# Optimization experiments

Measured on AMD Instinct MI355X. Metric: run time of the kernel, lower is better.

## Reference

```python
import jax, jax.numpy as jnp
import numpy as np

B, S, D = 4, 2048, 1024
E = 8            # num_experts
H = 2 * D        # int(4*D*(1/top_k)) with top_k=2, scaling_factor='auto'


def setup_inputs() -> dict:
    key = jax.random.key(0)
    ks = jax.random.split(key, 8)
    sd = 1.0 / np.sqrt(D)
    sh = 1.0 / np.sqrt(H)
    return {
        "x": jax.random.normal(ks[0], (B, S, D), dtype=jnp.float32),
        "top_k": 2,
        "Wg": jax.random.uniform(ks[1], (D, E), jnp.float32, -sd, sd),
        "bg": jax.random.uniform(ks[2], (E,), jnp.float32, -sd, sd),
        "W1": jax.random.uniform(ks[3], (E, D, H), jnp.float32, -sd, sd),
        "b1": jax.random.uniform(ks[4], (E, H), jnp.float32, -sd, sd),
        "W2": jax.random.uniform(ks[5], (E, H, D), jnp.float32, -sh, sh),
        "b2": jax.random.uniform(ks[6], (E, D), jnp.float32, -sh, sh),
    }


def reference(x, top_k, Wg, bg, W1, b1, W2, b2):
    b, s, d = x.shape
    e = W1.shape[0]
    T = b * s
    xt = x.reshape(T, d)                                   # [T, D]
    gate_logits = xt @ Wg + bg                             # [T, E]
    gate_probas = jax.nn.softmax(gate_logits, axis=-1)
    topk_p, topk_i = jax.lax.top_k(gate_probas, top_k)     # [T, K]
    topk_p = topk_p / jnp.sum(topk_p, axis=-1, keepdims=True)
    # combine weights per expert: zero for unselected experts
    w = jnp.zeros((T, e), dtype=x.dtype).at[jnp.arange(T)[:, None], topk_i].add(topk_p)  # [T, E]
    # dense grouped FFN over experts; unselected experts are zero-weighted,
    # so the weighted combine matches the original gather-MLP-scatter math
    h = jax.nn.gelu(jnp.einsum('td,edh->teh', xt, W1) + b1, approximate=True)  # [T, E, H]
    y = jnp.einsum('teh,ehd->ted', h, W2) + b2             # [T, E, D]
    out = jnp.einsum('te,ted->td', w, y)                   # [T, D]
    return out.reshape(b, s, d)
```

## Files before the change

### kernel.cpp

```cpp
#include <hip/hip_runtime.h>

typedef unsigned short u16;
typedef short v8s __attribute__((ext_vector_type(8)));
typedef float v4f __attribute__((ext_vector_type(4)));
typedef u16 u16x8 __attribute__((ext_vector_type(8)));
typedef u16 u16x4 __attribute__((ext_vector_type(4)));

constexpr int Tn = 8192;
constexpr int Dd = 1024;
constexpr int Hh = 2048;
constexpr int Ee = 8;
constexpr int MAXP = 17;

static __device__ __forceinline__ u16 f2bf(float v) {
  unsigned u = __float_as_uint(v);
  unsigned r = (u + 0x7fffu + ((u >> 16) & 1u)) >> 16;
  return (u16)r;
}

static __device__ __forceinline__ float bf2f(u16 v) {
  return __uint_as_float(((unsigned)v) << 16);
}

static __device__ __forceinline__ void gload_lds16(const u16* g, u16* l) {
  __builtin_amdgcn_global_load_lds(
      (const __attribute__((address_space(1))) unsigned int*)g,
      (__attribute__((address_space(3))) unsigned int*)l, 16, 0, 0);
}


__global__ __launch_bounds__(256) void prep_kernel(
    const float* __restrict__ x, const float* __restrict__ Wg, const float* __restrict__ bg,
    int* __restrict__ topki, float* __restrict__ topkw, u16* __restrict__ xb,
    const float* __restrict__ W1, u16* __restrict__ w1t,
    const float* __restrict__ W2, u16* __restrict__ w2t) {
  __shared__ float tile[64][65];
  int blk = blockIdx.x;

  if (blk < 2048) {
    int lane = threadIdx.x & 63;
    int t = blk * 4 + (threadIdx.x >> 6);
    const float4* xr = reinterpret_cast<const float4*>(x + (size_t)t * Dd);
    float acc[8] = {0.f, 0.f, 0.f, 0.f, 0.f, 0.f, 0.f, 0.f};
#pragma unroll
    for (int it = 0; it < 4; ++it) {
      float4 xv = xr[it * 64 + lane];
      int r = it * 256 + lane * 4;
      ushort4 o;
      o.x = f2bf(xv.x); o.y = f2bf(xv.y); o.z = f2bf(xv.z); o.w = f2bf(xv.w);
      *reinterpret_cast<ushort4*>(xb + (size_t)t * Dd + r) = o;
      const float4* wr = reinterpret_cast<const float4*>(Wg + (size_t)r * 8);
      float xs[4] = {xv.x, xv.y, xv.z, xv.w};
#pragma unroll
      for (int q = 0; q < 4; ++q) {
        float4 a = wr[q * 2], b = wr[q * 2 + 1];
        acc[0] += xs[q] * a.x; acc[1] += xs[q] * a.y; acc[2] += xs[q] * a.z; acc[3] += xs[q] * a.w;
        acc[4] += xs[q] * b.x; acc[5] += xs[q] * b.y; acc[6] += xs[q] * b.z; acc[7] += xs[q] * b.w;
      }
    }
#pragma unroll
    for (int e = 0; e < 8; ++e) {
#pragma unroll
      for (int off = 32; off > 0; off >>= 1) acc[e] += __shfl_xor(acc[e], off, 64);
    }
    if (lane == 0) {
      float l[8];
      float mx = -1e30f;
#pragma unroll
      for (int e = 0; e < 8; ++e) { l[e] = acc[e] + bg[e]; mx = fmaxf(mx, l[e]); }
      int i0 = 0;
#pragma unroll
      for (int e = 1; e < 8; ++e) if (l[e] > l[i0]) i0 = e;
      int i1 = (i0 == 0) ? 1 : 0;
#pragma unroll
      for (int e = 0; e < 8; ++e) if (e != i0 && l[e] > l[i1]) i1 = e;
      float e0 = __expf(l[i0] - mx), e1 = __expf(l[i1] - mx);
      float inv = 1.0f / (e0 + e1);
      topki[2 * t] = i0; topki[2 * t + 1] = i1;
      topkw[2 * t] = e0 * inv; topkw[2 * t + 1] = e1 * inv;
    }
    return;
  }

  int b = blk - 2048;
  bool isW1 = b < 4096;
  const float* in;
  u16* out;
  int R, C, cx, cy, e;
  if (isW1) {
    e = b >> 9;
    int t = b & 511;
    R = Dd; C = Hh; cx = t & 31; cy = t >> 5;
    in = W1; out = w1t;
  } else {
    int bb = b - 4096;
    e = bb >> 9;
    int t = bb & 511;
    R = Hh; C = Dd; cx = t & 15; cy = t >> 4;
    in = W2; out = w2t;
  }
  const float* ip = in + (size_t)e * Dd * Hh;
  u16* op = out + (size_t)e * Dd * Hh;
  int c0 = cx * 64, r0 = cy * 64;
  int tid = threadIdx.x;

#pragma unroll
  for (int k = 0; k < 4; ++k) {
    int f = k * 256 + tid;
    int r = f >> 4, c4 = (f & 15) * 4;
    float4 v = *reinterpret_cast<const float4*>(ip + (size_t)(r0 + r) * C + c0 + c4);
    tile[r][c4] = v.x; tile[r][c4 + 1] = v.y; tile[r][c4 + 2] = v.z; tile[r][c4 + 3] = v.w;
  }
  __syncthreads();

  int j = tid & 7;
#pragma unroll
  for (int rr = 0; rr < 2; ++rr) {
    int oc = (tid >> 3) + rr * 32;
    u16x8 o;
    if (isW1) {
#pragma unroll
      for (int q = 0; q < 8; ++q) o[q] = f2bf(tile[j * 8 + q][oc]);
    } else {
#pragma unroll
      for (int q = 0; q < 8; ++q) {
        int p = j * 8 + q;
        int src = (p & 3) * 16 + (p >> 2);
        o[q] = f2bf(tile[src][oc]);
      }
    }
    *reinterpret_cast<u16x8*>(op + (size_t)(c0 + oc) * R + r0 + j * 8) = o;
  }
}

__global__ __launch_bounds__(512) void sort_kernel(
    const int* __restrict__ topki,
    int* __restrict__ offs, int* __restrict__ rows, int* __restrict__ slotmap,
    int* __restrict__ panelE, int* __restrict__ panelB, int* __restrict__ nPanels) {
  __shared__ int scan[8][512];
  __shared__ int tot_l[8];
  __shared__ int offs_l[9];
  const int tt = threadIdx.x;
  const int base = tt * 32;

  int ev[32];
  int cnt[8] = {0, 0, 0, 0, 0, 0, 0, 0};
#pragma unroll
  for (int jj = 0; jj < 32; ++jj) {
    int e = topki[base + jj];
    ev[jj] = e;
#pragma unroll
    for (int q = 0; q < 8; ++q) cnt[q] += (e == q) ? 1 : 0;
  }
#pragma unroll
  for (int q = 0; q < 8; ++q) scan[q][tt] = cnt[q];
  __syncthreads();

  {
    int w = tt >> 6, l = tt & 63;
    int v[8];
    int s = 0;
#pragma unroll
    for (int jj = 0; jj < 8; ++jj) { v[jj] = scan[w][l * 8 + jj]; s += v[jj]; }
    int si = s;
#pragma unroll
    for (int off = 1; off < 64; off <<= 1) {
      int o = __shfl_up(si, off, 64);
      if (l >= off) si += o;
    }
    int run = si - s;
#pragma unroll
    for (int jj = 0; jj < 8; ++jj) { scan[w][l * 8 + jj] = run; run += v[jj]; }
    if (l == 63) tot_l[w] = si;
  }
  __syncthreads();

  if (tt == 0) {
    int o = 0;
#pragma unroll
    for (int e = 0; e < 8; ++e) { offs_l[e] = o; o += tot_l[e]; }
    offs_l[8] = o;
#pragma unroll
    for (int e = 0; e < 9; ++e) offs[e] = offs_l[e];
    int np = 0;
    for (int e = 0; e < 8; ++e) {
      for (int m0 = 0; m0 < tot_l[e]; m0 += 128) {
        panelE[np] = e;
        panelB[np] = offs_l[e] + m0;
        ++np;
      }
    }
    *nPanels = np;
  }
  __syncthreads();

#pragma unroll
  for (int jj = 0; jj < 32; ++jj) {
    int e = ev[jj];
    int idx = base + jj;
    int slot = scan[e][tt]++;
    slot += offs_l[e];
    rows[slot] = idx >> 1;
    slotmap[idx] = slot;
  }
}


__global__ __launch_bounds__(256, 2) void gemm1_kernel(
    const u16* __restrict__ xb, const u16* __restrict__ w1t, const float* __restrict__ b1,
    const int* __restrict__ offs, const int* __restrict__ rows,
    const int* __restrict__ panelE, const int* __restrict__ panelB,
    const int* __restrict__ nPanels, u16* __restrict__ hbuf) {
  const int bid = blockIdx.x;
  const int xcd = bid & 7;
  const int q = bid >> 3;
  const int n = q & 15;
  const int pi = (q >> 4) * 8 + xcd;
  if (pi >= *nPanels) return;
  const int e = panelE[pi];
  const int sbase = panelB[pi];
  const int lim = offs[e + 1];
  const int n0 = n * 128;

  __shared__ u16 As[128 * 64];
  __shared__ u16 Bs[128 * 64];

  const int tid = threadIdx.x;
  const int lane = tid & 63;
  const int wid = tid >> 6;
  const int wm = (wid >> 1) * 64;
  const int wn = (wid & 1) * 64;
  const int l16 = lane & 15;
  const int quad = lane >> 4;
  const int swz8 = (l16 & 7) * 8;

  const u16* aga[4];
  const u16* bga[4];
  u16* alds[4];
  u16* blds[4];
  const int lr = lane >> 3;
  const int g = (lane & 7) ^ (lr & 7);
  const int kcol = g * 8;
#pragma unroll
  for (int j = 0; j < 4; ++j) {
    int chunk = wid * 4 + j;
    int rowl = chunk * 8 + lr;
    int slot = sbase + rowl;
    if (slot >= lim) slot = sbase;
    aga[j] = xb + (size_t)rows[slot] * Dd + kcol;
    bga[j] = w1t + ((size_t)e * Hh + n0 + rowl) * Dd + kcol;
    alds[j] = As + chunk * 512;
    blds[j] = Bs + chunk * 512;
  }

  v4f acc[4][4];
#pragma unroll
  for (int i = 0; i < 4; ++i)
#pragma unroll
    for (int j = 0; j < 4; ++j) acc[i][j] = {0.f, 0.f, 0.f, 0.f};

  int rowAoff[4], rowBoff[4];
#pragma unroll
  for (int t_ = 0; t_ < 4; ++t_) {
    rowAoff[t_] = (wm + t_ * 16 + l16) * 64;
    rowBoff[t_] = (wn + t_ * 16 + l16) * 64;
  }

  for (int k0 = 0; k0 < Dd; k0 += 64) {
    __syncthreads();
#pragma unroll
    for (int j = 0; j < 4; ++j) gload_lds16(aga[j] + k0, alds[j]);
#pragma unroll
    for (int j = 0; j < 4; ++j) gload_lds16(bga[j] + k0, blds[j]);
    __syncthreads();

#pragma unroll
    for (int s = 0; s < 2; ++s) {
      int coff = ((s * 4 + quad) * 8) ^ swz8;
      v8s a[4], b[4];
#pragma unroll
      for (int mt = 0; mt < 4; ++mt)
        a[mt] = *reinterpret_cast<const v8s*>(&As[rowAoff[mt] + coff]);
#pragma unroll
      for (int nt = 0; nt < 4; ++nt)
        b[nt] = *reinterpret_cast<const v8s*>(&Bs[rowBoff[nt] + coff]);
#pragma unroll
      for (int mt = 0; mt < 4; ++mt)
#pragma unroll
        for (int nt = 0; nt < 4; ++nt)
          acc[mt][nt] = __builtin_amdgcn_mfma_f32_16x16x32_bf16(a[mt], b[nt], acc[mt][nt], 0, 0, 0);
    }
  }

  float b1v[4];
  const int ngbase = n0 + wn;
#pragma unroll
  for (int nt = 0; nt < 4; ++nt) b1v[nt] = b1[(size_t)e * Hh + ngbase + nt * 16 + l16];
#pragma unroll
  for (int mt = 0; mt < 4; ++mt) {
#pragma unroll
    for (int i = 0; i < 4; ++i) {
      int m = wm + mt * 16 + quad * 4 + i;
      if (sbase + m < lim) {
        u16x4 o;
#pragma unroll
        for (int nt = 0; nt < 4; ++nt) {
          float v = acc[mt][nt][i] + b1v[nt];
          float s = 1.0f / (1.0f + __expf(-1.5957691216057308f * (v + 0.044715f * v * v * v)));
          o[nt] = f2bf(v * s);
        }
        *reinterpret_cast<u16x4*>(hbuf + (size_t)(sbase + m) * Hh + ngbase + l16 * 4) = o;
      }
    }
  }
}

__global__ __launch_bounds__(256, 2) void gemm2_kernel(
    const u16* __restrict__ hbuf, const u16* __restrict__ w2t, const float* __restrict__ b2,
    const int* __restrict__ offs,
    const int* __restrict__ panelE, const int* __restrict__ panelB,
    const int* __restrict__ nPanels, u16* __restrict__ ybuf) {
  const int bid = blockIdx.x;
  const int xcd = bid & 7;
  const int q = bid >> 3;
  const int n = q & 7;
  const int pi = (q >> 3) * 8 + xcd;
  if (pi >= *nPanels) return;
  const int e = panelE[pi];
  const int sbase = panelB[pi];
  const int lim = offs[e + 1];
  const int n0 = n * 128;

  __shared__ u16 As[128 * 64];
  __shared__ u16 Bs[128 * 64];

  const int tid = threadIdx.x;
  const int lane = tid & 63;
  const int wid = tid >> 6;
  const int wm = (wid >> 1) * 64;
  const int wn = (wid & 1) * 64;
  const int l16 = lane & 15;
  const int quad = lane >> 4;
  const int swz8 = (l16 & 7) * 8;

  const u16* aga[4];
  const u16* bga[4];
  u16* alds[4];
  u16* blds[4];
  const int lr = lane >> 3;
  const int g = (lane & 7) ^ (lr & 7);
  const int kcol = g * 8;
#pragma unroll
  for (int j = 0; j < 4; ++j) {
    int chunk = wid * 4 + j;
    int rowl = chunk * 8 + lr;
    int slot = sbase + rowl;
    if (slot >= lim) slot = sbase;
    aga[j] = hbuf + (size_t)slot * Hh + kcol;
    bga[j] = w2t + ((size_t)e * Dd + n0 + rowl) * Hh + kcol;
    alds[j] = As + chunk * 512;
    blds[j] = Bs + chunk * 512;
  }

  v4f acc[4][4];
#pragma unroll
  for (int i = 0; i < 4; ++i)
#pragma unroll
    for (int j = 0; j < 4; ++j) acc[i][j] = {0.f, 0.f, 0.f, 0.f};

  int rowAoff[4], rowBoff[4];
#pragma unroll
  for (int t_ = 0; t_ < 4; ++t_) {
    rowAoff[t_] = (wm + t_ * 16 + l16) * 64;
    rowBoff[t_] = (wn + t_ * 16 + l16) * 64;
  }

  for (int k0 = 0; k0 < Hh; k0 += 64) {
    __syncthreads();
#pragma unroll
    for (int j = 0; j < 4; ++j) gload_lds16(aga[j] + k0, alds[j]);
#pragma unroll
    for (int j = 0; j < 4; ++j) gload_lds16(bga[j] + k0, blds[j]);
    __syncthreads();

#pragma unroll
    for (int s = 0; s < 2; ++s) {
      int coff = ((s * 4 + quad) * 8) ^ swz8;
      v8s a[4], b[4];
#pragma unroll
      for (int mt = 0; mt < 4; ++mt)
        a[mt] = *reinterpret_cast<const v8s*>(&As[rowAoff[mt] + coff]);
#pragma unroll
      for (int nt = 0; nt < 4; ++nt)
        b[nt] = *reinterpret_cast<const v8s*>(&Bs[rowBoff[nt] + coff]);
#pragma unroll
      for (int mt = 0; mt < 4; ++mt)
#pragma unroll
        for (int nt = 0; nt < 4; ++nt)
          acc[mt][nt] = __builtin_amdgcn_mfma_f32_16x16x32_bf16(a[mt], b[nt], acc[mt][nt], 0, 0, 0);
    }
  }

  float b2v[4];
  int ng[4];
#pragma unroll
  for (int nt = 0; nt < 4; ++nt) {
    ng[nt] = n0 + wn + nt * 16 + l16;
    b2v[nt] = b2[(size_t)e * Dd + ng[nt]];
  }
#pragma unroll
  for (int mt = 0; mt < 4; ++mt) {
#pragma unroll
    for (int i = 0; i < 4; ++i) {
      int m = wm + mt * 16 + quad * 4 + i;
      if (sbase + m < lim) {
        size_t rowbase = (size_t)(sbase + m) * Dd;
#pragma unroll
        for (int nt = 0; nt < 4; ++nt)
          ybuf[rowbase + ng[nt]] = f2bf(acc[mt][nt][i] + b2v[nt]);
      }
    }
  }
}

__global__ __launch_bounds__(256) void combine_kernel(
    const u16* __restrict__ ybuf, const int* __restrict__ slotmap,
    const float* __restrict__ topkw, float* __restrict__ out) {
  int idx = blockIdx.x * 256 + threadIdx.x;
  int t = idx >> 7;
  int d0 = (idx & 127) * 8;
  int s0 = slotmap[2 * t], s1 = slotmap[2 * t + 1];
  float w0 = topkw[2 * t], w1 = topkw[2 * t + 1];
  uint4 ya = *reinterpret_cast<const uint4*>(ybuf + (size_t)s0 * Dd + d0);
  uint4 yb = *reinterpret_cast<const uint4*>(ybuf + (size_t)s1 * Dd + d0);
  float r[8];
  const unsigned* pa = &ya.x;
  const unsigned* pb = &yb.x;
#pragma unroll
  for (int j = 0; j < 4; ++j) {
    unsigned a = pa[j], b = pb[j];
    r[2 * j]     = w0 * bf2f((u16)(a & 0xffff)) + w1 * bf2f((u16)(b & 0xffff));
    r[2 * j + 1] = w0 * bf2f((u16)(a >> 16))    + w1 * bf2f((u16)(b >> 16));
  }
  float4* op = reinterpret_cast<float4*>(out + (size_t)t * Dd + d0);
  op[0] = make_float4(r[0], r[1], r[2], r[3]);
  op[1] = make_float4(r[4], r[5], r[6], r[7]);
}

extern "C" void kernel_launch(void* const* d_in, const int* in_sizes, int n_in,
                              void* d_out, int out_size, void* d_ws, size_t ws_size,
                              hipStream_t stream) {
  const float* x  = (const float*)d_in[0];
  const float* Wg = (const float*)d_in[2];
  const float* bg = (const float*)d_in[3];
  const float* W1 = (const float*)d_in[4];
  const float* b1 = (const float*)d_in[5];
  const float* W2 = (const float*)d_in[6];
  const float* b2 = (const float*)d_in[7];
  float* out = (float*)d_out;

  char* p = (char*)d_ws;
  auto take = [&](size_t bytes) {
    char* q = p;
    p += (bytes + 255) & ~(size_t)255;
    return q;
  };
  int*   offs       = (int*)take(64);
  int*   panelE     = (int*)take(1024);
  int*   panelB     = (int*)take(1024);
  int*   nPanels    = (int*)take(256);
  int*   topki      = (int*)take((size_t)Tn * 2 * sizeof(int));
  float* topkw      = (float*)take((size_t)Tn * 2 * sizeof(float));
  int*   rows       = (int*)take((size_t)Tn * 2 * sizeof(int));
  int*   slotmap    = (int*)take((size_t)Tn * 2 * sizeof(int));
  u16*   xb         = (u16*)take((size_t)Tn * Dd * 2);
  u16*   w1t        = (u16*)take((size_t)Ee * Dd * Hh * 2);
  u16*   w2t        = (u16*)take((size_t)Ee * Dd * Hh * 2);
  u16*   hbuf       = (u16*)take((size_t)Tn * 2 * Hh * 2);
  u16*   ybuf       = (u16*)take((size_t)Tn * 2 * Dd * 2);

  prep_kernel<<<10240, 256, 0, stream>>>(x, Wg, bg, topki, topkw, xb, W1, w1t, W2, w2t);
  sort_kernel<<<1, 512, 0, stream>>>(topki, offs, rows, slotmap, panelE, panelB, nPanels);
  gemm1_kernel<<<8 * 16 * MAXP, 256, 0, stream>>>(xb, w1t, b1, offs, rows,
                                                  panelE, panelB, nPanels, hbuf);
  gemm2_kernel<<<8 * 8 * MAXP, 256, 0, stream>>>(hbuf, w2t, b2, offs,
                                                 panelE, panelB, nPanels, ybuf);
  combine_kernel<<<(Tn * Dd / 8) / 256, 256, 0, stream>>>(ybuf, slotmap, topkw, out);
}
```

Baseline: 428.6 us.

## Overlap W2 transpose with GEMM1 and scatter GEMM2 output to token order

```diff
diff --git a/kernel.cpp b/kernel.cpp
--- a/kernel.cpp
+++ b/kernel.cpp
@@ -11,6 +11,8 @@
 constexpr int Hh = 2048;
 constexpr int Ee = 8;
 constexpr int MAXP = 17;
+constexpr int G1GEMM = 8 * 16 * MAXP;
+constexpr int G1XTRA = 1024;
 
 static __device__ __forceinline__ u16 f2bf(float v) {
   unsigned u = __float_as_uint(v);
@@ -29,81 +31,10 @@
 }
 
 
-__global__ __launch_bounds__(256) void prep_kernel(
-    const float* __restrict__ x, const float* __restrict__ Wg, const float* __restrict__ bg,
-    int* __restrict__ topki, float* __restrict__ topkw, u16* __restrict__ xb,
-    const float* __restrict__ W1, u16* __restrict__ w1t,
-    const float* __restrict__ W2, u16* __restrict__ w2t) {
-  __shared__ float tile[64][65];
-  int blk = blockIdx.x;
-
-  if (blk < 2048) {
-    int lane = threadIdx.x & 63;
-    int t = blk * 4 + (threadIdx.x >> 6);
-    const float4* xr = reinterpret_cast<const float4*>(x + (size_t)t * Dd);
-    float acc[8] = {0.f, 0.f, 0.f, 0.f, 0.f, 0.f, 0.f, 0.f};
-#pragma unroll
-    for (int it = 0; it < 4; ++it) {
-      float4 xv = xr[it * 64 + lane];
-      int r = it * 256 + lane * 4;
-      ushort4 o;
-      o.x = f2bf(xv.x); o.y = f2bf(xv.y); o.z = f2bf(xv.z); o.w = f2bf(xv.w);
-      *reinterpret_cast<ushort4*>(xb + (size_t)t * Dd + r) = o;
-      const float4* wr = reinterpret_cast<const float4*>(Wg + (size_t)r * 8);
-      float xs[4] = {xv.x, xv.y, xv.z, xv.w};
-#pragma unroll
-      for (int q = 0; q < 4; ++q) {
-        float4 a = wr[q * 2], b = wr[q * 2 + 1];
-        acc[0] += xs[q] * a.x; acc[1] += xs[q] * a.y; acc[2] += xs[q] * a.z; acc[3] += xs[q] * a.w;
-        acc[4] += xs[q] * b.x; acc[5] += xs[q] * b.y; acc[6] += xs[q] * b.z; acc[7] += xs[q] * b.w;
-      }
-    }
-#pragma unroll
-    for (int e = 0; e < 8; ++e) {
-#pragma unroll
-      for (int off = 32; off > 0; off >>= 1) acc[e] += __shfl_xor(acc[e], off, 64);
-    }
-    if (lane == 0) {
-      float l[8];
-      float mx = -1e30f;
-#pragma unroll
-      for (int e = 0; e < 8; ++e) { l[e] = acc[e] + bg[e]; mx = fmaxf(mx, l[e]); }
-      int i0 = 0;
-#pragma unroll
-      for (int e = 1; e < 8; ++e) if (l[e] > l[i0]) i0 = e;
-      int i1 = (i0 == 0) ? 1 : 0;
-#pragma unroll
-      for (int e = 0; e < 8; ++e) if (e != i0 && l[e] > l[i1]) i1 = e;
-      float e0 = __expf(l[i0] - mx), e1 = __expf(l[i1] - mx);
-      float inv = 1.0f / (e0 + e1);
-      topki[2 * t] = i0; topki[2 * t + 1] = i1;
-      topkw[2 * t] = e0 * inv; topkw[2 * t + 1] = e1 * inv;
-    }
-    return;
-  }
-
-  int b = blk - 2048;
-  bool isW1 = b < 4096;
-  const float* in;
-  u16* out;
-  int R, C, cx, cy, e;
-  if (isW1) {
-    e = b >> 9;
-    int t = b & 511;
-    R = Dd; C = Hh; cx = t & 31; cy = t >> 5;
-    in = W1; out = w1t;
-  } else {
-    int bb = b - 4096;
-    e = bb >> 9;
-    int t = bb & 511;
-    R = Hh; C = Dd; cx = t & 15; cy = t >> 4;
-    in = W2; out = w2t;
-  }
-  const float* ip = in + (size_t)e * Dd * Hh;
-  u16* op = out + (size_t)e * Dd * Hh;
-  int c0 = cx * 64, r0 = cy * 64;
+static __device__ __forceinline__ void transpose_tile64(
+    const float* __restrict__ ip, u16* __restrict__ op,
+    int R, int C, int r0, int c0, bool permute, float (*tile)[65]) {
   int tid = threadIdx.x;
-
 #pragma unroll
   for (int k = 0; k < 4; ++k) {
     int f = k * 256 + tid;
@@ -112,20 +43,19 @@
     tile[r][c4] = v.x; tile[r][c4 + 1] = v.y; tile[r][c4 + 2] = v.z; tile[r][c4 + 3] = v.w;
   }
   __syncthreads();
-
   int j = tid & 7;
 #pragma unroll
   for (int rr = 0; rr < 2; ++rr) {
     int oc = (tid >> 3) + rr * 32;
     u16x8 o;
-    if (isW1) {
+    if (!permute) {
 #pragma unroll
       for (int q = 0; q < 8; ++q) o[q] = f2bf(tile[j * 8 + q][oc]);
     } else {
 #pragma unroll
       for (int q = 0; q < 8; ++q) {
-        int p = j * 8 + q;
-        int src = (p & 3) * 16 + (p >> 2);
+        int p_ = j * 8 + q;
+        int src = (p_ & 3) * 16 + (p_ >> 2);
         o[q] = f2bf(tile[src][oc]);
       }
     }
@@ -133,9 +63,69 @@
   }
 }
 
+__global__ __launch_bounds__(256) void prep_kernel(
+    const float* __restrict__ x, const float* __restrict__ Wg, const float* __restrict__ bg,
+    int* __restrict__ topki, float* __restrict__ topkw, u16* __restrict__ xb,
+    const float* __restrict__ W1, u16* __restrict__ w1t) {
+  __shared__ float tile[64][65];
+  int blk = blockIdx.x;
+
+  if (blk < 4096) {
+    int e = blk >> 9;
+    int t = blk & 511;
+    int cx = t & 31, cy = t >> 5;
+    const float* ip = W1 + (size_t)e * Dd * Hh;
+    u16* op = w1t + (size_t)e * Dd * Hh;
+    transpose_tile64(ip, op, Dd, Hh, cy * 64, cx * 64, false, tile);
+    return;
+  }
+
+  int lane = threadIdx.x & 63;
+  int t = (blk - 4096) * 4 + (threadIdx.x >> 6);
+  const float4* xr = reinterpret_cast<const float4*>(x + (size_t)t * Dd);
+  float acc[8] = {0.f, 0.f, 0.f, 0.f, 0.f, 0.f, 0.f, 0.f};
+#pragma unroll
+  for (int it = 0; it < 4; ++it) {
+    float4 xv = xr[it * 64 + lane];
+    int r = it * 256 + lane * 4;
+    ushort4 o;
+    o.x = f2bf(xv.x); o.y = f2bf(xv.y); o.z = f2bf(xv.z); o.w = f2bf(xv.w);
+    *reinterpret_cast<ushort4*>(xb + (size_t)t * Dd + r) = o;
+    const float4* wr = reinterpret_cast<const float4*>(Wg + (size_t)r * 8);
+    float xs[4] = {xv.x, xv.y, xv.z, xv.w};
+#pragma unroll
+    for (int q = 0; q < 4; ++q) {
+      float4 a = wr[q * 2], b = wr[q * 2 + 1];
+      acc[0] += xs[q] * a.x; acc[1] += xs[q] * a.y; acc[2] += xs[q] * a.z; acc[3] += xs[q] * a.w;
+      acc[4] += xs[q] * b.x; acc[5] += xs[q] * b.y; acc[6] += xs[q] * b.z; acc[7] += xs[q] * b.w;
+    }
+  }
+#pragma unroll
+  for (int e = 0; e < 8; ++e) {
+#pragma unroll
+    for (int off = 32; off > 0; off >>= 1) acc[e] += __shfl_xor(acc[e], off, 64);
+  }
+  if (lane == 0) {
+    float l[8];
+    float mx = -1e30f;
+#pragma unroll
+    for (int e = 0; e < 8; ++e) { l[e] = acc[e] + bg[e]; mx = fmaxf(mx, l[e]); }
+    int i0 = 0;
+#pragma unroll
+    for (int e = 1; e < 8; ++e) if (l[e] > l[i0]) i0 = e;
+    int i1 = (i0 == 0) ? 1 : 0;
+#pragma unroll
+    for (int e = 0; e < 8; ++e) if (e != i0 && l[e] > l[i1]) i1 = e;
+    float e0 = __expf(l[i0] - mx), e1 = __expf(l[i1] - mx);
+    float inv = 1.0f / (e0 + e1);
+    topki[2 * t] = i0; topki[2 * t + 1] = i1;
+    topkw[2 * t] = e0 * inv; topkw[2 * t + 1] = e1 * inv;
+  }
+}
+
 __global__ __launch_bounds__(512) void sort_kernel(
     const int* __restrict__ topki,
-    int* __restrict__ offs, int* __restrict__ rows, int* __restrict__ slotmap,
+    int* __restrict__ offs, int* __restrict__ rows,
     int* __restrict__ panelE, int* __restrict__ panelB, int* __restrict__ nPanels) {
   __shared__ int scan[8][512];
   __shared__ int tot_l[8];
@@ -198,10 +188,8 @@
   for (int jj = 0; jj < 32; ++jj) {
     int e = ev[jj];
     int idx = base + jj;
-    int slot = scan[e][tt]++;
-    slot += offs_l[e];
-    rows[slot] = idx >> 1;
-    slotmap[idx] = slot;
+    int slot = scan[e][tt]++ + offs_l[e];
+    rows[slot] = idx;
   }
 }
 
@@ -210,8 +198,29 @@
     const u16* __restrict__ xb, const u16* __restrict__ w1t, const float* __restrict__ b1,
     const int* __restrict__ offs, const int* __restrict__ rows,
     const int* __restrict__ panelE, const int* __restrict__ panelB,
-    const int* __restrict__ nPanels, u16* __restrict__ hbuf) {
+    const int* __restrict__ nPanels, u16* __restrict__ hbuf,
+    const float* __restrict__ W2, u16* __restrict__ w2t) {
+  __shared__ __align__(16) u16 smem[2 * 128 * 64];
+  u16* As = smem;
+  u16* Bs = smem + 128 * 64;
+
   const int bid = blockIdx.x;
+  if (bid >= G1GEMM) {
+    float (*tile)[65] = reinterpret_cast<float (*)[65]>(smem);
+    int tb = bid - G1GEMM;
+#pragma unroll 1
+    for (int s = 0; s < 4; ++s) {
+      int tileid = tb * 4 + s;
+      int e = tileid >> 9;
+      int t = tileid & 511;
+      int cx = t & 15, cy = t >> 4;
+      if (s) __syncthreads();
+      transpose_tile64(W2 + (size_t)e * Dd * Hh, w2t + (size_t)e * Dd * Hh,
+                       Hh, Dd, cy * 64, cx * 64, true, tile);
+    }
+    return;
+  }
+
   const int xcd = bid & 7;
   const int q = bid >> 3;
   const int n = q & 15;
@@ -222,9 +231,6 @@
   const int lim = offs[e + 1];
   const int n0 = n * 128;
 
-  __shared__ u16 As[128 * 64];
-  __shared__ u16 Bs[128 * 64];
-
   const int tid = threadIdx.x;
   const int lane = tid & 63;
   const int wid = tid >> 6;
@@ -247,7 +253,7 @@
     int rowl = chunk * 8 + lr;
     int slot = sbase + rowl;
     if (slot >= lim) slot = sbase;
-    aga[j] = xb + (size_t)rows[slot] * Dd + kcol;
+    aga[j] = xb + (size_t)(rows[slot] >> 1) * Dd + kcol;
     bga[j] = w1t + ((size_t)e * Hh + n0 + rowl) * Dd + kcol;
     alds[j] = As + chunk * 512;
     blds[j] = Bs + chunk * 512;
@@ -317,7 +323,7 @@
 
 __global__ __launch_bounds__(256, 2) void gemm2_kernel(
     const u16* __restrict__ hbuf, const u16* __restrict__ w2t, const float* __restrict__ b2,
-    const int* __restrict__ offs,
+    const int* __restrict__ offs, const int* __restrict__ rows,
     const int* __restrict__ panelE, const int* __restrict__ panelB,
     const int* __restrict__ nPanels, u16* __restrict__ ybuf) {
   const int bid = blockIdx.x;
@@ -331,8 +337,9 @@
   const int lim = offs[e + 1];
   const int n0 = n * 128;
 
-  __shared__ u16 As[128 * 64];
-  __shared__ u16 Bs[128 * 64];
+  __shared__ __align__(16) u16 smem[2 * 128 * 64];
+  u16* As = smem;
+  u16* Bs = smem + 128 * 64;
 
   const int tid = threadIdx.x;
   const int lane = tid & 63;
@@ -414,7 +421,7 @@
     for (int i = 0; i < 4; ++i) {
       int m = wm + mt * 16 + quad * 4 + i;
       if (sbase + m < lim) {
-        size_t rowbase = (size_t)(sbase + m) * Dd;
+        size_t rowbase = (size_t)rows[sbase + m] * Dd;
 #pragma unroll
         for (int nt = 0; nt < 4; ++nt)
           ybuf[rowbase + ng[nt]] = f2bf(acc[mt][nt][i] + b2v[nt]);
@@ -424,15 +431,14 @@
 }
 
 __global__ __launch_bounds__(256) void combine_kernel(
-    const u16* __restrict__ ybuf, const int* __restrict__ slotmap,
-    const float* __restrict__ topkw, float* __restrict__ out) {
+    const u16* __restrict__ ybuf, const float* __restrict__ topkw,
+    float* __restrict__ out) {
   int idx = blockIdx.x * 256 + threadIdx.x;
   int t = idx >> 7;
   int d0 = (idx & 127) * 8;
-  int s0 = slotmap[2 * t], s1 = slotmap[2 * t + 1];
   float w0 = topkw[2 * t], w1 = topkw[2 * t + 1];
-  uint4 ya = *reinterpret_cast<const uint4*>(ybuf + (size_t)s0 * Dd + d0);
-  uint4 yb = *reinterpret_cast<const uint4*>(ybuf + (size_t)s1 * Dd + d0);
+  uint4 ya = *reinterpret_cast<const uint4*>(ybuf + (size_t)(2 * t) * Dd + d0);
+  uint4 yb = *reinterpret_cast<const uint4*>(ybuf + (size_t)(2 * t + 1) * Dd + d0);
   float r[8];
   const unsigned* pa = &ya.x;
   const unsigned* pb = &yb.x;
@@ -472,18 +478,18 @@
   int*   topki      = (int*)take((size_t)Tn * 2 * sizeof(int));
   float* topkw      = (float*)take((size_t)Tn * 2 * sizeof(float));
   int*   rows       = (int*)take((size_t)Tn * 2 * sizeof(int));
-  int*   slotmap    = (int*)take((size_t)Tn * 2 * sizeof(int));
   u16*   xb         = (u16*)take((size_t)Tn * Dd * 2);
   u16*   w1t        = (u16*)take((size_t)Ee * Dd * Hh * 2);
   u16*   w2t        = (u16*)take((size_t)Ee * Dd * Hh * 2);
   u16*   hbuf       = (u16*)take((size_t)Tn * 2 * Hh * 2);
   u16*   ybuf       = (u16*)take((size_t)Tn * 2 * Dd * 2);
 
-  prep_kernel<<<10240, 256, 0, stream>>>(x, Wg, bg, topki, topkw, xb, W1, w1t, W2, w2t);
-  sort_kernel<<<1, 512, 0, stream>>>(topki, offs, rows, slotmap, panelE, panelB, nPanels);
-  gemm1_kernel<<<8 * 16 * MAXP, 256, 0, stream>>>(xb, w1t, b1, offs, rows,
-                                                  panelE, panelB, nPanels, hbuf);
-  gemm2_kernel<<<8 * 8 * MAXP, 256, 0, stream>>>(hbuf, w2t, b2, offs,
+  prep_kernel<<<6144, 256, 0, stream>>>(x, Wg, bg, topki, topkw, xb, W1, w1t);
+  sort_kernel<<<1, 512, 0, stream>>>(topki, offs, rows, panelE, panelB, nPanels);
+  gemm1_kernel<<<G1GEMM + G1XTRA, 256, 0, stream>>>(xb, w1t, b1, offs, rows,
+                                                    panelE, panelB, nPanels, hbuf,
+                                                    W2, w2t);
+  gemm2_kernel<<<8 * 8 * MAXP, 256, 0, stream>>>(hbuf, w2t, b2, offs, rows,
                                                  panelE, panelB, nPanels, ybuf);
-  combine_kernel<<<(Tn * Dd / 8) / 256, 256, 0, stream>>>(ybuf, slotmap, topkw, out);
-}
+  combine_kernel<<<(Tn * Dd / 8) / 256, 256, 0, stream>>>(ybuf, topkw, out);
+}
```

Result: faster. 410.9 us (-4.1%).
